# Performance work log

Measured on AMD Instinct MI355X. Metric: run time of the kernel, lower is better.

## Reference

```python
import jax, jax.numpy as jnp
import numpy as np

B, S, H, E, K = 4, 2048, 1024, 8, 2


def setup_inputs() -> dict:
    key = jax.random.key(0)
    k_hs, k_eo, k_w1, k_w2 = jax.random.split(key, 4)
    return {
        "hidden_states": jax.random.normal(k_hs, (B, S, H), dtype=jnp.float32),
        "expert_outputs": jax.random.normal(k_eo, (E, B, S, H), dtype=jnp.float32),
        "W1": jax.random.normal(k_w1, (H, H), dtype=jnp.float32) * 0.02,
        "b1": jnp.zeros((H,), dtype=jnp.float32),
        "W2": jax.random.normal(k_w2, (H, E), dtype=jnp.float32) * 0.02,
        "b2": jnp.zeros((E,), dtype=jnp.float32),
        "k": K,
    }


def reference(hidden_states, expert_outputs, W1, b1, W2, b2, k):
    # Router MLP (eval mode: dropout is identity, no noise)
    h = jax.nn.relu(hidden_states @ W1 + b1)          # [B,S,H]
    router_logits = h @ W2 + b2                        # [B,S,E]
    router_probs = jax.nn.softmax(router_logits, axis=-1)
    top_k_gates, top_k_indices = jax.lax.top_k(router_probs, k)  # [B,S,k]
    n_experts = expert_outputs.shape[0]
    # Scatter top-k gates into a dense [B,S,E] gate matrix (same math as the
    # per-expert masked accumulation in the torch loop)
    onehot = jax.nn.one_hot(top_k_indices, n_experts, dtype=top_k_gates.dtype)  # [B,S,k,E]
    gate_mat = jnp.einsum('bsk,bske->bse', top_k_gates, onehot)
    combined = jnp.einsum('bse,ebsd->bsd', gate_mat, expert_outputs)
    return combined
```

## Files before the change

kernel.cpp:

```cpp
#include <hip/hip_runtime.h>
#include <math.h>


#define H_DIM 1024
#define E_NUM 8

typedef __attribute__((ext_vector_type(8))) short s16x8;
typedef __attribute__((ext_vector_type(8))) unsigned short u16x8;
typedef __attribute__((ext_vector_type(4))) float f32x4;

__device__ __forceinline__ unsigned short f2bf(float x) {
    unsigned int u = __float_as_uint(x);
    unsigned int r = (u + 0x7FFFu + ((u >> 16) & 1u)) >> 16;
    return (unsigned short)r;
}
__device__ __forceinline__ float bf2f(unsigned short b) {
    return __uint_as_float(((unsigned int)b) << 16);
}

__device__ __forceinline__ void gload_lds16(const void* g, void* lds) {
    __builtin_amdgcn_global_load_lds(
        (const __attribute__((address_space(1))) void*)g,
        (__attribute__((address_space(3))) void*)lds, 16, 0, 0);
}

__global__ __launch_bounds__(256) void prep_a_kernel(
    const float* __restrict__ A, char* __restrict__ img)
{
    int t = blockIdx.x * 256 + threadIdx.x;
    int m = t >> 7;
    int k = (t & 127) << 3;
    const float* src = A + ((size_t)m << 10) + k;
    float4 v0 = *reinterpret_cast<const float4*>(src);
    float4 v1 = *reinterpret_cast<const float4*>(src + 4);
    float xs[8] = {v0.x, v0.y, v0.z, v0.w, v1.x, v1.y, v1.z, v1.w};
    u16x8 hv, lv;
    #pragma unroll
    for (int j = 0; j < 8; ++j) {
        unsigned short h = f2bf(xs[j]);
        hv[j] = h;
        lv[j] = f2bf(xs[j] - bf2f(h));
    }
    int rb = m >> 7, mr = m & 127, kt = k >> 5, s = (k >> 3) & 3;
    char* base = img + (((size_t)(rb * 32 + kt)) << 14) + mr * 128;
    *reinterpret_cast<u16x8*>(base + ((s ^ (mr & 7)) << 4)) = hv;
    *reinterpret_cast<u16x8*>(base + (((s + 4) ^ (mr & 7)) << 4)) = lv;
}

__global__ __launch_bounds__(256) void prep_b_kernel(
    const float* __restrict__ W, char* __restrict__ img)
{
    int t = blockIdx.x * 256 + threadIdx.x;
    int n = t & 1023;
    int k = (t >> 10) << 3;
    u16x8 hv, lv;
    #pragma unroll
    for (int j = 0; j < 8; ++j) {
        float x = W[((size_t)(k + j) << 10) + n];
        unsigned short h = f2bf(x);
        hv[j] = h;
        lv[j] = f2bf(x - bf2f(h));
    }
    int cb = n >> 7, nr = n & 127, kt = k >> 5, s = (k >> 3) & 3;
    char* base = img + (((size_t)(cb * 32 + kt)) << 14) + nr * 128;
    *reinterpret_cast<u16x8*>(base + ((s ^ (nr & 7)) << 4)) = hv;
    *reinterpret_cast<u16x8*>(base + (((s + 4) ^ (nr & 7)) << 4)) = lv;
}

__global__ __launch_bounds__(256, 2) void gemm1_mfma_kernel(
    const char* __restrict__ Aimg, const char* __restrict__ Bimg,
    const float* __restrict__ bias, float* __restrict__ Hout)
{
    __shared__ char As[16384];
    __shared__ char Bs[16384];

    int bid = blockIdx.x;
    int swz = (bid & 7) * 64 + (bid >> 3);
    int rb = swz >> 3;
    int cb = swz & 7;

    int tid = threadIdx.x;
    int lane = tid & 63;
    int wave = tid >> 6;
    int wm = (wave >> 1) * 64;
    int wn = (wave & 1) * 64;
    int l15 = lane & 15, l4 = lane >> 4;

    int aoff_h[4], aoff_l[4], boff_h[4], boff_l[4];
    #pragma unroll
    for (int f = 0; f < 4; ++f) {
        int ar = wm + f * 16 + l15;
        aoff_h[f] = ar * 128 + ((l4 ^ (ar & 7)) << 4);
        aoff_l[f] = ar * 128 + (((l4 + 4) ^ (ar & 7)) << 4);
        int br = wn + f * 16 + l15;
        boff_h[f] = br * 128 + ((l4 ^ (br & 7)) << 4);
        boff_l[f] = br * 128 + (((l4 + 4) ^ (br & 7)) << 4);
    }

    const char* abase = Aimg + (size_t)rb * (32 * 16384);
    const char* bbase = Bimg + (size_t)cb * (32 * 16384);

    f32x4 acc[4][4];
    #pragma unroll
    for (int i = 0; i < 4; ++i)
        #pragma unroll
        for (int j = 0; j < 4; ++j)
            acc[i][j] = (f32x4){0.f, 0.f, 0.f, 0.f};

    for (int kt = 0; kt < 32; ++kt) {
        const char* ga = abase + (kt << 14);
        const char* gb = bbase + (kt << 14);
        int toff = tid << 4;
        #pragma unroll
        for (int r = 0; r < 4; ++r) {
            gload_lds16(ga + (r << 12) + toff, As + (r << 12) + toff);
            gload_lds16(gb + (r << 12) + toff, Bs + (r << 12) + toff);
        }
        __syncthreads();

        s16x8 ah[4], al[4], bh[4], bl[4];
        #pragma unroll
        for (int f = 0; f < 4; ++f) {
            ah[f] = *reinterpret_cast<const s16x8*>(As + aoff_h[f]);
            al[f] = *reinterpret_cast<const s16x8*>(As + aoff_l[f]);
            bh[f] = *reinterpret_cast<const s16x8*>(Bs + boff_h[f]);
            bl[f] = *reinterpret_cast<const s16x8*>(Bs + boff_l[f]);
        }
        #pragma unroll
        for (int m = 0; m < 4; ++m)
            #pragma unroll
            for (int n = 0; n < 4; ++n) {
                acc[m][n] = __builtin_amdgcn_mfma_f32_16x16x32_bf16(ah[m], bh[n], acc[m][n], 0, 0, 0);
                acc[m][n] = __builtin_amdgcn_mfma_f32_16x16x32_bf16(ah[m], bl[n], acc[m][n], 0, 0, 0);
                acc[m][n] = __builtin_amdgcn_mfma_f32_16x16x32_bf16(al[m], bh[n], acc[m][n], 0, 0, 0);
            }
        __syncthreads();
    }

    int row0 = rb * 128 + wm;
    int col0 = cb * 128 + wn;
    float bcol[4];
    #pragma unroll
    for (int fn = 0; fn < 4; ++fn) bcol[fn] = bias[col0 + fn * 16 + l15];
    #pragma unroll
    for (int fm = 0; fm < 4; ++fm)
        #pragma unroll
        for (int r = 0; r < 4; ++r) {
            int row = row0 + fm * 16 + l4 * 4 + r;
            float* orow = Hout + ((size_t)row << 10);
            #pragma unroll
            for (int fn = 0; fn < 4; ++fn) {
                int col = col0 + fn * 16 + l15;
                orow[col] = fmaxf(acc[fm][fn][r] + bcol[fn], 0.f);
            }
        }
}

#define BM 128
#define BN 128
#define BK 16
#define PAD_LD 132

__global__ __launch_bounds__(256) void gemm1_relu_kernel(
    const float* __restrict__ A, const float* __restrict__ W,
    const float* __restrict__ bias, float* __restrict__ Hout,
    int M, int N, int K)
{
    __shared__ float As[BK][PAD_LD];
    __shared__ float Bs[BK][PAD_LD];
    const int tid = threadIdx.x;
    const int tx = tid & 15;
    const int ty = tid >> 4;
    const int row0 = blockIdx.y * BM;
    const int col0 = blockIdx.x * BN;
    float acc[8][8];
    #pragma unroll
    for (int i = 0; i < 8; ++i)
        #pragma unroll
        for (int j = 0; j < 8; ++j) acc[i][j] = 0.f;
    const int a_row = tid >> 2;
    const int a_k4  = (tid & 3) * 4;
    const int b_col4 = (tid & 31) * 4;
    const int b_kk   = tid >> 5;
    for (int k0 = 0; k0 < K; k0 += BK) {
        #pragma unroll
        for (int half = 0; half < 2; ++half) {
            int r = a_row + half * 64;
            float4 av = *reinterpret_cast<const float4*>(&A[(size_t)(row0 + r) * K + k0 + a_k4]);
            As[a_k4 + 0][r] = av.x; As[a_k4 + 1][r] = av.y;
            As[a_k4 + 2][r] = av.z; As[a_k4 + 3][r] = av.w;
        }
        #pragma unroll
        for (int half = 0; half < 2; ++half) {
            int kk = b_kk + half * 8;
            float4 bv = *reinterpret_cast<const float4*>(&W[(size_t)(k0 + kk) * N + col0 + b_col4]);
            *reinterpret_cast<float4*>(&Bs[kk][b_col4]) = bv;
        }
        __syncthreads();
        #pragma unroll
        for (int k = 0; k < BK; ++k) {
            float4 a0 = *reinterpret_cast<const float4*>(&As[k][ty * 8]);
            float4 a1 = *reinterpret_cast<const float4*>(&As[k][ty * 8 + 4]);
            float4 b0 = *reinterpret_cast<const float4*>(&Bs[k][tx * 8]);
            float4 b1 = *reinterpret_cast<const float4*>(&Bs[k][tx * 8 + 4]);
            float a[8] = {a0.x, a0.y, a0.z, a0.w, a1.x, a1.y, a1.z, a1.w};
            float b[8] = {b0.x, b0.y, b0.z, b0.w, b1.x, b1.y, b1.z, b1.w};
            #pragma unroll
            for (int i = 0; i < 8; ++i)
                #pragma unroll
                for (int j = 0; j < 8; ++j)
                    acc[i][j] = fmaf(a[i], b[j], acc[i][j]);
        }
        __syncthreads();
    }
    #pragma unroll
    for (int i = 0; i < 8; ++i) {
        int row = row0 + ty * 8 + i;
        #pragma unroll
        for (int j4 = 0; j4 < 2; ++j4) {
            int col = col0 + tx * 8 + j4 * 4;
            float4 v;
            v.x = fmaxf(acc[i][j4 * 4 + 0] + bias[col + 0], 0.f);
            v.y = fmaxf(acc[i][j4 * 4 + 1] + bias[col + 1], 0.f);
            v.z = fmaxf(acc[i][j4 * 4 + 2] + bias[col + 2], 0.f);
            v.w = fmaxf(acc[i][j4 * 4 + 3] + bias[col + 3], 0.f);
            *reinterpret_cast<float4*>(&Hout[(size_t)row * N + col]) = v;
        }
    }
}

__global__ __launch_bounds__(256) void route_combine_kernel(
    const float* __restrict__ Hbuf, const float* __restrict__ W2,
    const float* __restrict__ b2, const float* __restrict__ EO,
    float* __restrict__ Out, int M)
{
    const int t = blockIdx.x;
    const int tid = threadIdx.x;
    const int lane = tid & 63;
    const int wave = tid >> 6;
    const float* hrow = Hbuf + (size_t)t * H_DIM;

    float part[E_NUM];
    #pragma unroll
    for (int e = 0; e < E_NUM; ++e) part[e] = 0.f;
    #pragma unroll
    for (int it = 0; it < H_DIM / 256; ++it) {
        int j = tid + it * 256;
        float hv = hrow[j];
        const float* w = W2 + (size_t)j * E_NUM;
        #pragma unroll
        for (int e = 0; e < E_NUM; ++e) part[e] = fmaf(hv, w[e], part[e]);
    }
    #pragma unroll
    for (int off = 32; off > 0; off >>= 1)
        #pragma unroll
        for (int e = 0; e < E_NUM; ++e)
            part[e] += __shfl_down(part[e], off, 64);

    __shared__ float sred[4][E_NUM];
    __shared__ float s_g[2];
    __shared__ int   s_e[2];
    if (lane == 0)
        #pragma unroll
        for (int e = 0; e < E_NUM; ++e) sred[wave][e] = part[e];
    __syncthreads();

    if (tid == 0) {
        float logits[E_NUM];
        #pragma unroll
        for (int e = 0; e < E_NUM; ++e)
            logits[e] = sred[0][e] + sred[1][e] + sred[2][e] + sred[3][e] + b2[e];
        float m = logits[0];
        #pragma unroll
        for (int e = 1; e < E_NUM; ++e) m = fmaxf(m, logits[e]);
        float p[E_NUM], ssum = 0.f;
        #pragma unroll
        for (int e = 0; e < E_NUM; ++e) { p[e] = expf(logits[e] - m); ssum += p[e]; }
        float inv = 1.f / ssum;
        #pragma unroll
        for (int e = 0; e < E_NUM; ++e) p[e] *= inv;
        int e0 = 0;
        #pragma unroll
        for (int e = 1; e < E_NUM; ++e) if (p[e] > p[e0]) e0 = e;
        int e1 = (e0 == 0) ? 1 : 0;
        #pragma unroll
        for (int e = 0; e < E_NUM; ++e)
            if (e != e0 && e != e1 && p[e] > p[e1]) e1 = e;
        s_g[0] = p[e0]; s_g[1] = p[e1];
        s_e[0] = e0;    s_e[1] = e1;
    }
    __syncthreads();

    const float g0 = s_g[0], g1 = s_g[1];
    const size_t base0 = ((size_t)s_e[0] * M + t) * H_DIM;
    const size_t base1 = ((size_t)s_e[1] * M + t) * H_DIM;
    const int d = tid * 4;
    float4 x0 = *reinterpret_cast<const float4*>(&EO[base0 + d]);
    float4 x1 = *reinterpret_cast<const float4*>(&EO[base1 + d]);
    float4 o;
    o.x = g0 * x0.x + g1 * x1.x;
    o.y = g0 * x0.y + g1 * x1.y;
    o.z = g0 * x0.z + g1 * x1.z;
    o.w = g0 * x0.w + g1 * x1.w;
    *reinterpret_cast<float4*>(&Out[(size_t)t * H_DIM + d]) = o;
}

extern "C" void kernel_launch(void* const* d_in, const int* in_sizes, int n_in,
                              void* d_out, int out_size, void* d_ws, size_t ws_size,
                              hipStream_t stream)
{
    const float* hs = (const float*)d_in[0];
    const float* EO = (const float*)d_in[1];
    const float* W1 = (const float*)d_in[2];
    const float* b1 = (const float*)d_in[3];
    const float* W2 = (const float*)d_in[4];
    const float* b2 = (const float*)d_in[5];

    const int M = in_sizes[0] / H_DIM;
    float* out = (float*)d_out;

    const size_t A_IMG = (size_t)64 * 32 * 16384;
    const size_t B_IMG = (size_t)8 * 32 * 16384;
    if (M == 8192 && ws_size >= A_IMG + B_IMG) {
        char* Aimg = (char*)d_ws;
        char* Bimg = (char*)d_ws + A_IMG;
        prep_a_kernel<<<4096, 256, 0, stream>>>(hs, Aimg);
        prep_b_kernel<<<512, 256, 0, stream>>>(W1, Bimg);
        gemm1_mfma_kernel<<<512, 256, 0, stream>>>(Aimg, Bimg, b1, out);
    } else {
        dim3 grid1(H_DIM / BN, M / BM);
        gemm1_relu_kernel<<<grid1, 256, 0, stream>>>(hs, W1, b1, out, M, H_DIM, H_DIM);
    }
    route_combine_kernel<<<M, 256, 0, stream>>>(out, W2, b2, EO, out, M);
}
```

Baseline: 88.10 us.

## Double-buffer GEMM1 with 256x128 tiles, 8 waves, and fuse prep kernels

The two bf16-split prep kernels are merged into one launch that branches on block index. The router GEMM kernel now uses 512-thread blocks computing 256x128 tiles, so each B tile is reused across two A row blocks. K-tiles are double-buffered in 96KB of LDS, with the next tile prefetched before the current one is computed, and raw s_waitcnt/s_barrier calls replace __syncthreads. MFMA phases are split by barriers and s_setprio. The aim is to hide global-load latency, reuse B more, and save one launch, at the cost of more LDS per block, which may cut occupancy, and more fragile hand-written synchronisation.

```diff
diff --git a/kernel.cpp b/kernel.cpp
--- a/kernel.cpp
+++ b/kernel.cpp
@@ -17,88 +17,97 @@
 __device__ __forceinline__ float bf2f(unsigned short b) {
     return __uint_as_float(((unsigned int)b) << 16);
 }
-
 __device__ __forceinline__ void gload_lds16(const void* g, void* lds) {
     __builtin_amdgcn_global_load_lds(
         (const __attribute__((address_space(1))) void*)g,
         (__attribute__((address_space(3))) void*)lds, 16, 0, 0);
 }
 
-__global__ __launch_bounds__(256) void prep_a_kernel(
-    const float* __restrict__ A, char* __restrict__ img)
-{
-    int t = blockIdx.x * 256 + threadIdx.x;
-    int m = t >> 7;
-    int k = (t & 127) << 3;
-    const float* src = A + ((size_t)m << 10) + k;
-    float4 v0 = *reinterpret_cast<const float4*>(src);
-    float4 v1 = *reinterpret_cast<const float4*>(src + 4);
-    float xs[8] = {v0.x, v0.y, v0.z, v0.w, v1.x, v1.y, v1.z, v1.w};
-    u16x8 hv, lv;
-    #pragma unroll
-    for (int j = 0; j < 8; ++j) {
-        unsigned short h = f2bf(xs[j]);
-        hv[j] = h;
-        lv[j] = f2bf(xs[j] - bf2f(h));
-    }
-    int rb = m >> 7, mr = m & 127, kt = k >> 5, s = (k >> 3) & 3;
-    char* base = img + (((size_t)(rb * 32 + kt)) << 14) + mr * 128;
-    *reinterpret_cast<u16x8*>(base + ((s ^ (mr & 7)) << 4)) = hv;
-    *reinterpret_cast<u16x8*>(base + (((s + 4) ^ (mr & 7)) << 4)) = lv;
-}
-
-__global__ __launch_bounds__(256) void prep_b_kernel(
-    const float* __restrict__ W, char* __restrict__ img)
-{
-    int t = blockIdx.x * 256 + threadIdx.x;
-    int n = t & 1023;
-    int k = (t >> 10) << 3;
-    u16x8 hv, lv;
-    #pragma unroll
-    for (int j = 0; j < 8; ++j) {
-        float x = W[((size_t)(k + j) << 10) + n];
-        unsigned short h = f2bf(x);
-        hv[j] = h;
-        lv[j] = f2bf(x - bf2f(h));
-    }
-    int cb = n >> 7, nr = n & 127, kt = k >> 5, s = (k >> 3) & 3;
-    char* base = img + (((size_t)(cb * 32 + kt)) << 14) + nr * 128;
-    *reinterpret_cast<u16x8*>(base + ((s ^ (nr & 7)) << 4)) = hv;
-    *reinterpret_cast<u16x8*>(base + (((s + 4) ^ (nr & 7)) << 4)) = lv;
-}
-
-__global__ __launch_bounds__(256, 2) void gemm1_mfma_kernel(
+__global__ __launch_bounds__(256) void prep_fused_kernel(
+    const float* __restrict__ A, const float* __restrict__ W,
+    char* __restrict__ Aimg, char* __restrict__ Bimg)
+{
+    if (blockIdx.x < 4096) {
+        int t = blockIdx.x * 256 + threadIdx.x;
+        int m = t >> 7;
+        int k = (t & 127) << 3;
+        const float* src = A + ((size_t)m << 10) + k;
+        float4 v0 = *reinterpret_cast<const float4*>(src);
+        float4 v1 = *reinterpret_cast<const float4*>(src + 4);
+        float xs[8] = {v0.x, v0.y, v0.z, v0.w, v1.x, v1.y, v1.z, v1.w};
+        u16x8 hv, lv;
+        #pragma unroll
+        for (int j = 0; j < 8; ++j) {
+            unsigned short h = f2bf(xs[j]);
+            hv[j] = h;
+            lv[j] = f2bf(xs[j] - bf2f(h));
+        }
+        int rb = m >> 7, mr = m & 127, kt = k >> 5, s = (k >> 3) & 3;
+        char* base = Aimg + (((size_t)(rb * 32 + kt)) << 14) + mr * 128;
+        *reinterpret_cast<u16x8*>(base + ((s ^ (mr & 7)) << 4)) = hv;
+        *reinterpret_cast<u16x8*>(base + (((s + 4) ^ (mr & 7)) << 4)) = lv;
+    } else {
+        int t = (blockIdx.x - 4096) * 256 + threadIdx.x;
+        int n = t & 1023;
+        int k = (t >> 10) << 3;
+        u16x8 hv, lv;
+        #pragma unroll
+        for (int j = 0; j < 8; ++j) {
+            float x = W[((size_t)(k + j) << 10) + n];
+            unsigned short h = f2bf(x);
+            hv[j] = h;
+            lv[j] = f2bf(x - bf2f(h));
+        }
+        int cb = n >> 7, nr = n & 127, kt = k >> 5, s = (k >> 3) & 3;
+        char* base = Bimg + (((size_t)(cb * 32 + kt)) << 14) + nr * 128;
+        *reinterpret_cast<u16x8*>(base + ((s ^ (nr & 7)) << 4)) = hv;
+        *reinterpret_cast<u16x8*>(base + (((s + 4) ^ (nr & 7)) << 4)) = lv;
+    }
+}
+
+#define MFMA_B16 __builtin_amdgcn_mfma_f32_16x16x32_bf16
+
+__global__ __launch_bounds__(512, 2) void gemm1_mfma8_kernel(
     const char* __restrict__ Aimg, const char* __restrict__ Bimg,
     const float* __restrict__ bias, float* __restrict__ Hout)
 {
-    __shared__ char As[16384];
-    __shared__ char Bs[16384];
-
-    int bid = blockIdx.x;
-    int swz = (bid & 7) * 64 + (bid >> 3);
-    int rb = swz >> 3;
-    int cb = swz & 7;
-
-    int tid = threadIdx.x;
-    int lane = tid & 63;
-    int wave = tid >> 6;
-    int wm = (wave >> 1) * 64;
-    int wn = (wave & 1) * 64;
-    int l15 = lane & 15, l4 = lane >> 4;
+    __shared__ char smem[98304];
+
+    const int bid = blockIdx.x;
+    const int swz = (bid & 7) * 32 + (bid >> 3);
+    const int rb2 = swz >> 3;
+    const int cb  = swz & 7;
+
+    const int tid = threadIdx.x;
+    const int lane = tid & 63;
+    const int wave = tid >> 6;
+    const int wm = (wave >> 1) * 64;
+    const int wn = (wave & 1) * 64;
+    const int l15 = lane & 15, l4 = lane >> 4;
+    const int toff = tid << 4;
 
     int aoff_h[4], aoff_l[4], boff_h[4], boff_l[4];
     #pragma unroll
     for (int f = 0; f < 4; ++f) {
         int ar = wm + f * 16 + l15;
-        aoff_h[f] = ar * 128 + ((l4 ^ (ar & 7)) << 4);
-        aoff_l[f] = ar * 128 + (((l4 + 4) ^ (ar & 7)) << 4);
+        aoff_h[f] = ((ar >> 7) << 14) + (ar & 127) * 128 + ((l4 ^ (ar & 7)) << 4);
+        aoff_l[f] = ((ar >> 7) << 14) + (ar & 127) * 128 + (((l4 + 4) ^ (ar & 7)) << 4);
         int br = wn + f * 16 + l15;
         boff_h[f] = br * 128 + ((l4 ^ (br & 7)) << 4);
         boff_l[f] = br * 128 + (((l4 + 4) ^ (br & 7)) << 4);
     }
 
-    const char* abase = Aimg + (size_t)rb * (32 * 16384);
-    const char* bbase = Bimg + (size_t)cb * (32 * 16384);
+    const char* gA = Aimg + (((size_t)(rb2 * 2) * 32) << 14);
+    const char* gB = Bimg + (((size_t)cb * 32) << 14);
+
+#define STAGE(aOfs, bOfs, kt_) do {                                                         \
+    gload_lds16(gA + (((size_t)(kt_)) << 14) + toff,            smem + (aOfs) + toff);          \
+    gload_lds16(gA + (((size_t)(kt_)) << 14) + 8192 + toff,     smem + (aOfs) + 8192 + toff);   \
+    gload_lds16(gA + (((size_t)(32 + (kt_))) << 14) + toff,         smem + (aOfs) + 16384 + toff); \
+    gload_lds16(gA + (((size_t)(32 + (kt_))) << 14) + 8192 + toff,  smem + (aOfs) + 24576 + toff); \
+    gload_lds16(gB + (((size_t)(kt_)) << 14) + toff,            smem + (bOfs) + toff);          \
+    gload_lds16(gB + (((size_t)(kt_)) << 14) + 8192 + toff,     smem + (bOfs) + 8192 + toff);   \
+} while (0)
 
     f32x4 acc[4][4];
     #pragma unroll
@@ -107,38 +116,68 @@
         for (int j = 0; j < 4; ++j)
             acc[i][j] = (f32x4){0.f, 0.f, 0.f, 0.f};
 
+    STAGE(0, 65536, 0);
+
     for (int kt = 0; kt < 32; ++kt) {
-        const char* ga = abase + (kt << 14);
-        const char* gb = bbase + (kt << 14);
-        int toff = tid << 4;
-        #pragma unroll
-        for (int r = 0; r < 4; ++r) {
-            gload_lds16(ga + (r << 12) + toff, As + (r << 12) + toff);
-            gload_lds16(gb + (r << 12) + toff, Bs + (r << 12) + toff);
-        }
-        __syncthreads();
-
-        s16x8 ah[4], al[4], bh[4], bl[4];
+        const int cur = kt & 1;
+        const int aO = cur * 32768;
+        const int bO = 65536 + cur * 16384;
+        const char* curA = smem + aO;
+        const char* curB = smem + bO;
+        if (kt < 31) {
+            STAGE(aO ^ 32768, (bO ^ 16384), kt + 1);
+            asm volatile("s_waitcnt vmcnt(6)" ::: "memory");
+        } else {
+            asm volatile("s_waitcnt vmcnt(0)" ::: "memory");
+        }
+        asm volatile("s_barrier" ::: "memory");
+
+        s16x8 bh[4], bl[4];
         #pragma unroll
         for (int f = 0; f < 4; ++f) {
-            ah[f] = *reinterpret_cast<const s16x8*>(As + aoff_h[f]);
-            al[f] = *reinterpret_cast<const s16x8*>(As + aoff_l[f]);
-            bh[f] = *reinterpret_cast<const s16x8*>(Bs + boff_h[f]);
-            bl[f] = *reinterpret_cast<const s16x8*>(Bs + boff_l[f]);
-        }
-        #pragma unroll
-        for (int m = 0; m < 4; ++m)
-            #pragma unroll
-            for (int n = 0; n < 4; ++n) {
-                acc[m][n] = __builtin_amdgcn_mfma_f32_16x16x32_bf16(ah[m], bh[n], acc[m][n], 0, 0, 0);
-                acc[m][n] = __builtin_amdgcn_mfma_f32_16x16x32_bf16(ah[m], bl[n], acc[m][n], 0, 0, 0);
-                acc[m][n] = __builtin_amdgcn_mfma_f32_16x16x32_bf16(al[m], bh[n], acc[m][n], 0, 0, 0);
-            }
-        __syncthreads();
-    }
-
-    int row0 = rb * 128 + wm;
-    int col0 = cb * 128 + wn;
+            bh[f] = *reinterpret_cast<const s16x8*>(curB + boff_h[f]);
+            bl[f] = *reinterpret_cast<const s16x8*>(curB + boff_l[f]);
+        }
+        s16x8 a0h = *reinterpret_cast<const s16x8*>(curA + aoff_h[0]);
+        s16x8 a0l = *reinterpret_cast<const s16x8*>(curA + aoff_l[0]);
+        s16x8 a1h = *reinterpret_cast<const s16x8*>(curA + aoff_h[1]);
+        s16x8 a1l = *reinterpret_cast<const s16x8*>(curA + aoff_l[1]);
+        asm volatile("s_barrier" ::: "memory");
+        __builtin_amdgcn_s_setprio(1);
+        #pragma unroll
+        for (int n = 0; n < 4; ++n) {
+            acc[0][n] = MFMA_B16(a0h, bh[n], acc[0][n], 0, 0, 0);
+            acc[0][n] = MFMA_B16(a0h, bl[n], acc[0][n], 0, 0, 0);
+            acc[0][n] = MFMA_B16(a0l, bh[n], acc[0][n], 0, 0, 0);
+            acc[1][n] = MFMA_B16(a1h, bh[n], acc[1][n], 0, 0, 0);
+            acc[1][n] = MFMA_B16(a1h, bl[n], acc[1][n], 0, 0, 0);
+            acc[1][n] = MFMA_B16(a1l, bh[n], acc[1][n], 0, 0, 0);
+        }
+        __builtin_amdgcn_s_setprio(0);
+        asm volatile("s_barrier" ::: "memory");
+
+        s16x8 a2h = *reinterpret_cast<const s16x8*>(curA + aoff_h[2]);
+        s16x8 a2l = *reinterpret_cast<const s16x8*>(curA + aoff_l[2]);
+        s16x8 a3h = *reinterpret_cast<const s16x8*>(curA + aoff_h[3]);
+        s16x8 a3l = *reinterpret_cast<const s16x8*>(curA + aoff_l[3]);
+        asm volatile("s_barrier" ::: "memory");
+        __builtin_amdgcn_s_setprio(1);
+        #pragma unroll
+        for (int n = 0; n < 4; ++n) {
+            acc[2][n] = MFMA_B16(a2h, bh[n], acc[2][n], 0, 0, 0);
+            acc[2][n] = MFMA_B16(a2h, bl[n], acc[2][n], 0, 0, 0);
+            acc[2][n] = MFMA_B16(a2l, bh[n], acc[2][n], 0, 0, 0);
+            acc[3][n] = MFMA_B16(a3h, bh[n], acc[3][n], 0, 0, 0);
+            acc[3][n] = MFMA_B16(a3h, bl[n], acc[3][n], 0, 0, 0);
+            acc[3][n] = MFMA_B16(a3l, bh[n], acc[3][n], 0, 0, 0);
+        }
+        __builtin_amdgcn_s_setprio(0);
+        asm volatile("s_barrier" ::: "memory");
+    }
+#undef STAGE
+
+    const int row0 = rb2 * 256 + wm;
+    const int col0 = cb * 128 + wn;
     float bcol[4];
     #pragma unroll
     for (int fn = 0; fn < 4; ++fn) bcol[fn] = bias[col0 + fn * 16 + l15];
@@ -324,9 +363,8 @@
     if (M == 8192 && ws_size >= A_IMG + B_IMG) {
         char* Aimg = (char*)d_ws;
         char* Bimg = (char*)d_ws + A_IMG;
-        prep_a_kernel<<<4096, 256, 0, stream>>>(hs, Aimg);
-        prep_b_kernel<<<512, 256, 0, stream>>>(W1, Bimg);
-        gemm1_mfma_kernel<<<512, 256, 0, stream>>>(Aimg, Bimg, b1, out);
+        prep_fused_kernel<<<4096 + 512, 256, 0, stream>>>(hs, W1, Aimg, Bimg);
+        gemm1_mfma8_kernel<<<256, 512, 0, stream>>>(Aimg, Bimg, b1, out);
     } else {
         dim3 grid1(H_DIM / BN, M / BM);
         gemm1_relu_kernel<<<grid1, 256, 0, stream>>>(hs, W1, b1, out, M, H_DIM, H_DIM);
```

After: 90.88 us. +3.2%, slower.
